# Kernel tuning notes

Measured on AMD Instinct MI355X. Metric: run time of the kernel, lower is better.

The kernel has to match this reference:

```python
import jax, jax.numpy as jnp
import numpy as np
import math

H = 16  # n_head
DK = 64  # d_k = n_feat // n_head
BASE = 10000.0


def _rope_cos_sin(T, dk, dtype):
    inv_freq = 1.0 / (BASE ** (jnp.arange(0, dk, 2, dtype=jnp.float32) / dk))
    t = jnp.arange(T, dtype=jnp.float32)
    freqs = jnp.einsum('i,j->ij', t, inv_freq)          # [T, dk/2]
    emb = jnp.concatenate([freqs, freqs], axis=-1)       # [T, dk]
    return jnp.cos(emb).astype(dtype)[:, None, None, :], jnp.sin(emb).astype(dtype)[:, None, None, :]


def _rotate_half(x):
    x1, x2 = jnp.split(x, 2, axis=-1)
    return jnp.concatenate([-x2, x1], axis=-1)


def setup_inputs() -> dict:
    key = jax.random.key(0)
    ks = jax.random.split(key, 8)
    T, B, C = 2048, 2, 1024
    s = 0.02
    return {
        'query': jax.random.normal(ks[0], (T, B, C), jnp.float32),
        'key': jax.random.normal(ks[1], (T, B, C), jnp.float32),
        'value': jax.random.normal(ks[2], (T, B, C), jnp.float32),
        'Wq': jax.random.normal(ks[3], (C, C), jnp.float32) * s,
        'bq': jnp.zeros((C,), jnp.float32),
        'Wk': jax.random.normal(ks[4], (C, C), jnp.float32) * s,
        'bk': jnp.zeros((C,), jnp.float32),
        'Wv': jax.random.normal(ks[5], (C, C), jnp.float32) * s,
        'bv': jnp.zeros((C,), jnp.float32),
        'Wo': jax.random.normal(ks[6], (C, C), jnp.float32) * s,
        'bo': jnp.zeros((C,), jnp.float32),
    }


def reference(query, key, value, Wq, bq, Wk, bk, Wv, bv, Wo, bo):
    T, B, C = value.shape
    # --- RoPE applied to raw inputs (per the original module), before projections ---
    q = query.reshape(T, B, H, DK)
    k = key.reshape(T, B, H, DK)
    cos, sin = _rope_cos_sin(T, DK, q.dtype)  # [T,1,1,DK]
    q = q * cos + _rotate_half(q) * sin
    k = k * cos + _rotate_half(k) * sin
    q = q.reshape(T, B, C).transpose(1, 0, 2)   # [B,T,C]
    k = k.reshape(T, B, C).transpose(1, 0, 2)
    v = value.transpose(1, 0, 2)
    # --- QKV projections (torch Linear: x @ W.T + b) ---
    q = (jnp.einsum('btc,dc->btd', q, Wq) + bq).reshape(B, T, H, DK).transpose(0, 2, 1, 3)
    k = (jnp.einsum('btc,dc->btd', k, Wk) + bk).reshape(B, T, H, DK).transpose(0, 2, 1, 3)
    v = (jnp.einsum('btc,dc->btd', v, Wv) + bv).reshape(B, T, H, DK).transpose(0, 2, 1, 3)
    # --- scaled dot-product attention ---
    scores = jnp.einsum('bhqd,bhkd->bhqk', q, k) / math.sqrt(DK)
    attn = jax.nn.softmax(scores, axis=-1)
    x = jnp.einsum('bhqk,bhkd->bhqd', attn, v)        # [B,H,T,DK]
    x = x.transpose(0, 2, 1, 3).reshape(B, T, C)
    out = jnp.einsum('btc,dc->btd', x, Wo) + bo        # [B,T,C]
    return out.transpose(1, 0, 2)                      # [T,B,C]
```

## Files before the change

### kernel.cpp

```cpp
#include <hip/hip_runtime.h>
#include <hip/hip_bf16.h>
#include <math.h>

#define T_SEQ 2048
#define B_SZ 2
#define C_DIM 1024
#define H_HEADS 16
#define DKH 64
#define M_ROWS (T_SEQ * B_SZ)

#define QSCALE 0.1803368801111204f

typedef __attribute__((ext_vector_type(8))) short bf16x8;
typedef __attribute__((ext_vector_type(4))) float f32x4;
typedef unsigned short ushort_t;


__device__ __forceinline__ ushort_t f2bf(float f) {
    unsigned u = __float_as_uint(f);
    u += 0x7fffu + ((u >> 16) & 1u);
    return (ushort_t)(u >> 16);
}

__device__ __forceinline__ unsigned pack2bf(float a, float b) {
#if __has_builtin(__builtin_amdgcn_cvt_pk_bf16_f32)
    typedef __attribute__((ext_vector_type(2))) __bf16 bf16x2_t;
    union { bf16x2_t v; unsigned u; } cv;
    cv.v = __builtin_amdgcn_cvt_pk_bf16_f32(a, b);
    return cv.u;
#else
    return (unsigned)f2bf(a) | ((unsigned)f2bf(b) << 16);
#endif
}

__device__ __forceinline__ void async_copy16(const void* g, void* l) {
    __builtin_amdgcn_global_load_lds(
        (const __attribute__((address_space(1))) void*)g,
        (__attribute__((address_space(3))) void*)l, 16, 0, 0);
}

__global__ __launch_bounds__(256) void rope_cast_qk(
        const float* __restrict__ q, const float* __restrict__ k,
        ushort_t* __restrict__ qb, ushort_t* __restrict__ kb) {
    int idx  = blockIdx.x * 256 + threadIdx.x;
    int j    = idx & 31;
    int rest = idx >> 5;
    int h    = rest & (H_HEADS - 1);
    int tb   = rest >> 4;
    int t    = tb >> 1;
    float inv = exp2f(-(float)j * 0.41524101186092034f);
    float ang = (float)t * inv;
    float s, c;
    sincosf(ang, &s, &c);
    int base = tb * C_DIM + h * DKH + j;
    float q1 = q[base], q2 = q[base + 32];
    float k1 = k[base], k2 = k[base + 32];
    qb[base]      = f2bf(q1 * c - q2 * s);
    qb[base + 32] = f2bf(q2 * c + q1 * s);
    kb[base]      = f2bf(k1 * c - k2 * s);
    kb[base + 32] = f2bf(k2 * c + k1 * s);
}

__global__ __launch_bounds__(256) void cast_bf16_w4(
        const float* __restrict__ w0, const float* __restrict__ w1,
        const float* __restrict__ w2, const float* __restrict__ w3,
        ushort_t* __restrict__ o0, ushort_t* __restrict__ o1,
        ushort_t* __restrict__ o2, ushort_t* __restrict__ o3) {
    int which = blockIdx.y;
    const float* in = which == 0 ? w0 : which == 1 ? w1 : which == 2 ? w2 : w3;
    ushort_t*   out = which == 0 ? o0 : which == 1 ? o1 : which == 2 ? o2 : o3;
    int i = blockIdx.x * 256 + threadIdx.x;
    float4 v = reinterpret_cast<const float4*>(in)[i];
    ushort4 o;
    o.x = f2bf(v.x); o.y = f2bf(v.y); o.z = f2bf(v.z); o.w = f2bf(v.w);
    reinterpret_cast<ushort4*>(out)[i] = o;
}

__global__ __launch_bounds__(256) void cast_value_perm(
        const float* __restrict__ in, ushort_t* __restrict__ out) {
    int i   = blockIdx.x * 256 + threadIdx.x;
    int c4  = i & 255;
    int row = i >> 8;
    int b   = row >> 11, t = row & 2047;
    float4 v = reinterpret_cast<const float4*>(in)[(t * 2 + b) * 256 + c4];
    ushort4 o;
    o.x = f2bf(v.x); o.y = f2bf(v.y); o.z = f2bf(v.z); o.w = f2bf(v.w);
    reinterpret_cast<ushort4*>(out)[i] = o;
}

template <bool BF16_OUT, bool BIAS_ROW>
__global__ __launch_bounds__(512) void gemm_nt(
        const ushort_t* __restrict__ A, const ushort_t* __restrict__ W,
        const float* __restrict__ bias, void* __restrict__ Cout,
        int M, int N, int K, float scale) {
    __shared__ ushort_t As[128 * 64];
    __shared__ ushort_t Bs[64 * 64];
    const int tid  = threadIdx.x;
    const int lane = tid & 63;
    const int w    = tid >> 6;
    const int m16  = lane & 15, quad = lane >> 4;
    const int r8   = lane >> 3, c8 = lane & 7;
    const int clog = c8 ^ r8;
    const int rowBase = blockIdx.y * 128;
    const int colBase = blockIdx.x * 64;

    f32x4 acc[4];
#pragma unroll
    for (int j = 0; j < 4; j++) acc[j] = (f32x4){0.f, 0.f, 0.f, 0.f};

    for (int kt = 0; kt < K; kt += 64) {
        __syncthreads();
#pragma unroll
        for (int i = 0; i < 2; ++i) {
            int R = w * 16 + i * 8;
            async_copy16(A + (size_t)(rowBase + R + r8) * K + kt + clog * 8,
                         &As[R * 64]);
        }
        {
            int R = w * 8;
            async_copy16(W + (size_t)(colBase + R + r8) * K + kt + clog * 8,
                         &Bs[R * 64]);
        }
        __syncthreads();
#pragma unroll
        for (int ks = 0; ks < 2; ++ks) {
            int lc = ks * 4 + quad;
            bf16x8 af;
            {
                int R = w * 16 + m16;
                af = *reinterpret_cast<const bf16x8*>(
                    &As[R * 64 + ((lc ^ (R & 7)) << 3)]);
            }
            bf16x8 bfr[4];
#pragma unroll
            for (int ni = 0; ni < 4; ni++) {
                int R = ni * 16 + m16;
                bfr[ni] = *reinterpret_cast<const bf16x8*>(
                    &Bs[R * 64 + ((lc ^ (R & 7)) << 3)]);
            }
#pragma unroll
            for (int ni = 0; ni < 4; ni++)
                acc[ni] = __builtin_amdgcn_mfma_f32_16x16x32_bf16(
                    af, bfr[ni], acc[ni], 0, 0, 0);
        }
    }
#pragma unroll
    for (int ni = 0; ni < 4; ni++)
#pragma unroll
        for (int r = 0; r < 4; r++) {
            int row = rowBase + w * 16 + quad * 4 + r;
            int col = colBase + ni * 16 + m16;
            float v = (acc[ni][r] + (BIAS_ROW ? bias[row] : bias[col])) * scale;
            if (BF16_OUT)
                ((ushort_t*)Cout)[(size_t)row * N + col] = f2bf(v);
            else
                ((float*)Cout)[(size_t)row * N + col] = v;
        }
}

__global__ __launch_bounds__(256) void attn(
        const ushort_t* __restrict__ Qp, const ushort_t* __restrict__ Kp,
        const ushort_t* __restrict__ VTg, ushort_t* __restrict__ X) {
    __shared__ char smem[40960];
    ushort_t* Qt = (ushort_t*)smem;
    char*  KtC   = smem + 8192;
    char*  VTC   = smem + 24576;
    float* exch  = (float*)(smem + 8192);
    float* lbuf  = (float*)smem;

    const int tid  = threadIdx.x;
    const int lane = tid & 63;
    const int w    = tid >> 6;
    const int m16  = lane & 15, quad = lane >> 4;
    const int r8   = lane >> 3, c8 = lane & 7;
    const int clog = c8 ^ r8;

    const int lid   = blockIdx.x + blockIdx.y * 32;
    const int jj    = lid >> 3;
    const int pair  = (lid & 7) * 4 + (jj >> 5);
    const int qBase = (jj & 31) * 64;
    const int b = pair >> 4, h = pair & 15;

    const int ofA = m16 * 128 + ((quad ^ (m16 & 7)) << 4);
    const int ofB = m16 * 128 + (((4 + quad) ^ (m16 & 7)) << 4);
    const int sw4 = (m16 >> 1) & 3;
    const int fro = m16 * 64 + ((quad ^ sw4) << 4);
    int pw0[2];
#pragma unroll
    for (int kt_i = 0; kt_i < 2; kt_i++)
        pw0[kt_i] = m16 * 64 + (((kt_i * 2 + (quad >> 1)) ^ sw4) << 4) + (quad & 1) * 8;
    char* PwC = KtC + w * 4096;

    const int vlc = (lane & 3) ^ ((lane >> 3) & 3);

#pragma unroll
    for (int i = 0; i < 2; ++i) {
        int R = w * 16 + i * 8;
        async_copy16(Qp + (size_t)((qBase + R + r8) * 2 + b) * C_DIM + h * DKH + clog * 8,
                     &Qt[R * 64]);
    }
    __syncthreads();
    bf16x8 aq[4][2];
#pragma unroll
    for (int ni = 0; ni < 4; ni++) {
        aq[ni][0] = *reinterpret_cast<const bf16x8*>((const char*)Qt + ni * 2048 + ofA);
        aq[ni][1] = *reinterpret_cast<const bf16x8*>((const char*)Qt + ni * 2048 + ofB);
    }
    asm volatile("s_waitcnt lgkmcnt(0)" ::: "memory");
    __syncthreads();

    float lrun[4] = {0.f, 0.f, 0.f, 0.f};
    f32x4 o[4][4];
#pragma unroll
    for (int mi = 0; mi < 4; mi++)
#pragma unroll
        for (int ni = 0; ni < 4; ni++) o[mi][ni] = (f32x4){0.f, 0.f, 0.f, 0.f};

    auto stageKV = [&](int kt) {
#pragma unroll
        for (int i = 0; i < 4; ++i) {
            int key = kt + w * 32 + i * 8 + r8;
            async_copy16(Kp + (size_t)(key * 2 + b) * C_DIM + h * DKH + clog * 8,
                         KtC + w * 4096 + i * 1024);
        }
#pragma unroll
        for (int i = 0; i < 4; ++i) {
            int dkr = i * 16 + (lane >> 2);
            async_copy16(VTg + (size_t)(h * DKH + dkr) * M_ROWS + b * T_SEQ + kt + w * 32 + vlc * 8,
                         VTC + w * 4096 + i * 1024);
        }
    };

    stageKV(0);
    for (int kt = 0; kt < T_SEQ; kt += 128) {
        asm volatile("s_waitcnt vmcnt(0)" ::: "memory");
        __builtin_amdgcn_sched_barrier(0);

        f32x4 s[2][4];
#pragma unroll
        for (int kt_i = 0; kt_i < 2; kt_i++) {
#pragma unroll
            for (int ni = 0; ni < 4; ni++) s[kt_i][ni] = (f32x4){0.f, 0.f, 0.f, 0.f};
            bf16x8 kf0 = *reinterpret_cast<const bf16x8*>(KtC + w * 4096 + kt_i * 2048 + ofA);
            bf16x8 kf1 = *reinterpret_cast<const bf16x8*>(KtC + w * 4096 + kt_i * 2048 + ofB);
#pragma unroll
            for (int ni = 0; ni < 4; ni++) {
                s[kt_i][ni] = __builtin_amdgcn_mfma_f32_16x16x32_bf16(kf0, aq[ni][0], s[kt_i][ni], 0, 0, 0);
                s[kt_i][ni] = __builtin_amdgcn_mfma_f32_16x16x32_bf16(kf1, aq[ni][1], s[kt_i][ni], 0, 0, 0);
            }
        }

#pragma unroll
        for (int kt_i = 0; kt_i < 2; kt_i++)
#pragma unroll
            for (int ni = 0; ni < 4; ni++) {
                float p0 = __builtin_amdgcn_exp2f(s[kt_i][ni][0]);
                float p1 = __builtin_amdgcn_exp2f(s[kt_i][ni][1]);
                float p2 = __builtin_amdgcn_exp2f(s[kt_i][ni][2]);
                float p3 = __builtin_amdgcn_exp2f(s[kt_i][ni][3]);
                lrun[ni] += (p0 + p1) + (p2 + p3);
                uint2 pv;
                pv.x = pack2bf(p0, p1);
                pv.y = pack2bf(p2, p3);
                *reinterpret_cast<uint2*>(PwC + ni * 1024 + pw0[kt_i]) = pv;
            }
        asm volatile("s_waitcnt lgkmcnt(0)" ::: "memory");

        bf16x8 pf[4];
#pragma unroll
        for (int ni = 0; ni < 4; ni++)
            pf[ni] = *reinterpret_cast<const bf16x8*>(PwC + ni * 1024 + fro);
        bf16x8 vfr[4];
#pragma unroll
        for (int mi = 0; mi < 4; mi++)
            vfr[mi] = *reinterpret_cast<const bf16x8*>(VTC + w * 4096 + mi * 1024 + fro);
        asm volatile("s_waitcnt lgkmcnt(0)" ::: "memory");
        __builtin_amdgcn_sched_barrier(0);
        if (kt + 128 < T_SEQ) stageKV(kt + 128);
        __builtin_amdgcn_sched_barrier(0);

#pragma unroll
        for (int mi = 0; mi < 4; mi++)
#pragma unroll
            for (int ni = 0; ni < 4; ni++)
                o[mi][ni] = __builtin_amdgcn_mfma_f32_16x16x32_bf16(vfr[mi], pf[ni], o[mi][ni], 0, 0, 0);
    }

#pragma unroll
    for (int ni = 0; ni < 4; ni++) {
        lrun[ni] += __shfl_xor(lrun[ni], 16);
        lrun[ni] += __shfl_xor(lrun[ni], 32);
    }
    float lv = quad == 0 ? lrun[0] : quad == 1 ? lrun[1] : quad == 2 ? lrun[2] : lrun[3];
    lbuf[w * 64 + quad * 16 + m16] = lv;

    __syncthreads();

#pragma unroll
    for (int rnd = 0; rnd < 2; rnd++) {
        if (rnd) __syncthreads();
#pragma unroll
        for (int t2 = 0; t2 < 2; t2++) {
            int mi = 2 * rnd + t2;
#pragma unroll
            for (int ni = 0; ni < 4; ni++) {
                int q = ni * 16 + m16;
                int cw = t2 * 4 + quad;
                *reinterpret_cast<f32x4*>(
                    &exch[w * 2048 + q * 32 + ((cw ^ (q & 7)) << 2)]) = o[mi][ni];
            }
        }
        __syncthreads();
        int q = tid >> 2;
        float lsum = lbuf[q] + lbuf[64 + q] + lbuf[128 + q] + lbuf[192 + q];
        float invl = 1.0f / lsum;
#pragma unroll
        for (int half = 0; half < 2; half++) {
            int c = (tid & 3) + 4 * half;
            int off = q * 32 + (((c ^ (q & 7))) << 2);
            f32x4 v = *reinterpret_cast<const f32x4*>(&exch[off]);
            f32x4 v1 = *reinterpret_cast<const f32x4*>(&exch[2048 + off]);
            f32x4 v2 = *reinterpret_cast<const f32x4*>(&exch[4096 + off]);
            f32x4 v3 = *reinterpret_cast<const f32x4*>(&exch[6144 + off]);
            v = v + v1 + v2 + v3;
            uint2 pk;
            pk.x = pack2bf(v[0] * invl, v[1] * invl);
            pk.y = pack2bf(v[2] * invl, v[3] * invl);
            int t = qBase + q;
            *reinterpret_cast<uint2*>(
                &X[(size_t)(t * 2 + b) * C_DIM + h * DKH + rnd * 32 + c * 4]) = pk;
        }
    }
}

extern "C" void kernel_launch(void* const* d_in, const int* in_sizes, int n_in,
                              void* d_out, int out_size, void* d_ws, size_t ws_size,
                              hipStream_t stream) {
    const float* query = (const float*)d_in[0];
    const float* key   = (const float*)d_in[1];
    const float* value = (const float*)d_in[2];
    const float* Wq = (const float*)d_in[3];
    const float* bq = (const float*)d_in[4];
    const float* Wk = (const float*)d_in[5];
    const float* bk = (const float*)d_in[6];
    const float* Wv = (const float*)d_in[7];
    const float* bv = (const float*)d_in[8];
    const float* Wo = (const float*)d_in[9];
    const float* bo = (const float*)d_in[10];
    float* out = (float*)d_out;

    ushort_t* qb  = (ushort_t*)d_ws;
    ushort_t* kb  = qb  + (size_t)M_ROWS * C_DIM;
    ushort_t* vb2 = kb  + (size_t)M_ROWS * C_DIM;
    ushort_t* Wqb = vb2 + (size_t)M_ROWS * C_DIM;
    ushort_t* Wkb = Wqb + (size_t)C_DIM * C_DIM;
    ushort_t* Wvb = Wkb + (size_t)C_DIM * C_DIM;
    ushort_t* Wob = Wvb + (size_t)C_DIM * C_DIM;
    ushort_t* Qp  = Wob + (size_t)C_DIM * C_DIM;
    ushort_t* Kp  = Qp  + (size_t)M_ROWS * C_DIM;
    ushort_t* VTg = Kp  + (size_t)M_ROWS * C_DIM;
    ushort_t* Xb  = VTg + (size_t)M_ROWS * C_DIM;

    rope_cast_qk<<<(T_SEQ * B_SZ * H_HEADS * 32) / 256, 256, 0, stream>>>(query, key, qb, kb);
    cast_value_perm<<<(M_ROWS * C_DIM / 4) / 256, 256, 0, stream>>>(value, vb2);
    dim3 cg((C_DIM * C_DIM / 4) / 256, 4);
    cast_bf16_w4<<<cg, 256, 0, stream>>>(Wq, Wk, Wv, Wo, Wqb, Wkb, Wvb, Wob);

    dim3 gg(C_DIM / 64, M_ROWS / 128);
    gemm_nt<true, false><<<gg, 512, 0, stream>>>(qb, Wqb, bq, Qp, M_ROWS, C_DIM, C_DIM, QSCALE);
    gemm_nt<true, false><<<gg, 512, 0, stream>>>(kb, Wkb, bk, Kp, M_ROWS, C_DIM, C_DIM, 1.0f);
    dim3 gv(M_ROWS / 64, C_DIM / 128);
    gemm_nt<true, true><<<gv, 512, 0, stream>>>(Wvb, vb2, bv, VTg, C_DIM, M_ROWS, C_DIM, 1.0f);

    attn<<<dim3(T_SEQ / 64, B_SZ * H_HEADS), 256, 0, stream>>>(Qp, Kp, VTg, Xb);

    gemm_nt<false, false><<<gg, 512, 0, stream>>>(Xb, Wob, bo, (void*)out, M_ROWS, C_DIM, C_DIM, 1.0f);
}
```

Measured before the change: 240.6 us.

## Double-buffer GEMM LDS tiles and split attention K/V waits

```diff
diff --git a/kernel.cpp b/kernel.cpp
--- a/kernel.cpp
+++ b/kernel.cpp
@@ -93,8 +93,8 @@
         const ushort_t* __restrict__ A, const ushort_t* __restrict__ W,
         const float* __restrict__ bias, void* __restrict__ Cout,
         int M, int N, int K, float scale) {
-    __shared__ ushort_t As[128 * 64];
-    __shared__ ushort_t Bs[64 * 64];
+    __shared__ ushort_t As[2][128 * 64];
+    __shared__ ushort_t Bs[2][64 * 64];
     const int tid  = threadIdx.x;
     const int lane = tid & 63;
     const int w    = tid >> 6;
@@ -108,20 +108,33 @@
 #pragma unroll
     for (int j = 0; j < 4; j++) acc[j] = (f32x4){0.f, 0.f, 0.f, 0.f};
 
-    for (int kt = 0; kt < K; kt += 64) {
-        __syncthreads();
+    auto stage = [&](int buf, int kt) {
 #pragma unroll
         for (int i = 0; i < 2; ++i) {
             int R = w * 16 + i * 8;
             async_copy16(A + (size_t)(rowBase + R + r8) * K + kt + clog * 8,
-                         &As[R * 64]);
+                         &As[buf][R * 64]);
         }
         {
             int R = w * 8;
             async_copy16(W + (size_t)(colBase + R + r8) * K + kt + clog * 8,
-                         &Bs[R * 64]);
-        }
-        __syncthreads();
+                         &Bs[buf][R * 64]);
+        }
+    };
+
+    stage(0, 0);
+    int cur = 0;
+    for (int kt = 0; kt < K; kt += 64, cur ^= 1) {
+        if (kt + 64 < K) {
+            stage(cur ^ 1, kt + 64);
+            asm volatile("s_waitcnt vmcnt(3)" ::: "memory");
+        } else {
+            asm volatile("s_waitcnt vmcnt(0)" ::: "memory");
+        }
+        __builtin_amdgcn_s_barrier();
+        __builtin_amdgcn_sched_barrier(0);
+        const ushort_t* Asc = As[cur];
+        const ushort_t* Bsc = Bs[cur];
 #pragma unroll
         for (int ks = 0; ks < 2; ++ks) {
             int lc = ks * 4 + quad;
@@ -129,20 +142,21 @@
             {
                 int R = w * 16 + m16;
                 af = *reinterpret_cast<const bf16x8*>(
-                    &As[R * 64 + ((lc ^ (R & 7)) << 3)]);
+                    &Asc[R * 64 + ((lc ^ (R & 7)) << 3)]);
             }
             bf16x8 bfr[4];
 #pragma unroll
             for (int ni = 0; ni < 4; ni++) {
                 int R = ni * 16 + m16;
                 bfr[ni] = *reinterpret_cast<const bf16x8*>(
-                    &Bs[R * 64 + ((lc ^ (R & 7)) << 3)]);
+                    &Bsc[R * 64 + ((lc ^ (R & 7)) << 3)]);
             }
 #pragma unroll
             for (int ni = 0; ni < 4; ni++)
                 acc[ni] = __builtin_amdgcn_mfma_f32_16x16x32_bf16(
                     af, bfr[ni], acc[ni], 0, 0, 0);
         }
+        __builtin_amdgcn_s_barrier();
     }
 #pragma unroll
     for (int ni = 0; ni < 4; ni++)
@@ -233,7 +247,7 @@
 
     stageKV(0);
     for (int kt = 0; kt < T_SEQ; kt += 128) {
-        asm volatile("s_waitcnt vmcnt(0)" ::: "memory");
+        asm volatile("s_waitcnt vmcnt(4)" ::: "memory");
         __builtin_amdgcn_sched_barrier(0);
 
         f32x4 s[2][4];
@@ -270,6 +284,8 @@
 #pragma unroll
         for (int ni = 0; ni < 4; ni++)
             pf[ni] = *reinterpret_cast<const bf16x8*>(PwC + ni * 1024 + fro);
+        asm volatile("s_waitcnt vmcnt(0)" ::: "memory");
+        __builtin_amdgcn_sched_barrier(0);
         bf16x8 vfr[4];
 #pragma unroll
         for (int mi = 0; mi < 4; mi++)
```

Measured after the change: 240.2 us. About the same (-0.1%).
